# Optimization experiments

Measured on AMD Instinct MI355X. Metric: run time of the kernel, lower is better.

The kernel has to match this reference:

```python
import jax, jax.numpy as jnp
import numpy as np

B, T, C = 4, 4096, 512
H = 64           # head_size
GRAN = 128       # staircase granularity


def staircase_mask(t, g):
    # tril OR block-diagonal blocks of size g (the staircase fills the upper
    # triangle inside each gxg diagonal block)
    i = jnp.arange(t)
    return (i[:, None] >= i[None, :]) | ((i[:, None] // g) == (i[None, :] // g))


def setup_inputs() -> dict:
    key = jax.random.key(0)
    kx, kk, kq, kv = jax.random.split(key, 4)
    scale = 0.02
    return {
        "x": jax.random.normal(kx, (B, T, C), dtype=jnp.float32),
        "Wk": jax.random.normal(kk, (C, H), dtype=jnp.float32) * scale,
        "Wq": jax.random.normal(kq, (C, H), dtype=jnp.float32) * scale,
        "Wv": jax.random.normal(kv, (C, H), dtype=jnp.float32) * scale,
    }


def reference(x, Wk, Wq, Wv):
    # single head of self-attention with staircase mask (dropout off / eval mode)
    k = x @ Wk          # [B,T,H]
    q = x @ Wq          # [B,T,H]
    v = x @ Wv          # [B,T,H]
    wei = jnp.einsum("bth,bsh->bts", q, k) * (H ** -0.5)   # [B,T,T]
    mask = staircase_mask(T, GRAN)                           # [T,T] bool
    wei = jnp.where(mask, wei, -jnp.inf)
    wei = jax.nn.softmax(wei, axis=-1)
    out = jnp.einsum("bts,bsh->bth", wei, v)                 # [B,T,H]
    return out
```

## Files before the change

kernel.cpp:

```cpp
#include <hip/hip_runtime.h>

typedef unsigned short u16;
typedef unsigned int u32;
typedef unsigned long long u64;
typedef __attribute__((ext_vector_type(8))) short short8;
typedef __attribute__((ext_vector_type(4))) float f32x4;

#define T_ 4096

#if __has_builtin(__builtin_amdgcn_exp2f)
#define EXP2F(x) __builtin_amdgcn_exp2f(x)
#else
#define EXP2F(x) exp2f(x)
#endif

__device__ __forceinline__ u16 f2bf(float f) {
    unsigned u = __float_as_uint(f);
    u += 0x7FFFu + ((u >> 16) & 1u);
    return (u16)(u >> 16);
}

__global__ __launch_bounds__(256) void wtrans_kernel(
    const float* __restrict__ Wq, const float* __restrict__ Wk,
    const float* __restrict__ Wv, u16* __restrict__ WTf)
{
    const int tid  = blockIdx.x * 256 + threadIdx.x;
    const int frag = tid >> 6;
    const int lane = tid & 63;
    const int ng   = frag >> 4;
    const int kc   = frag & 15;
    const int m    = ng >> 2;
    const float* W = (m == 0) ? Wq : (m == 1) ? Wk : Wv;
    const int h  = (ng & 3) * 16 + (lane & 15);
    const int c0 = kc * 32 + (lane >> 4) * 8;
    short8 v;
    #pragma unroll
    for (int j = 0; j < 8; ++j)
        v[j] = (short)f2bf(W[(c0 + j) * 64 + h]);
    *(short8*)(WTf + (size_t)frag * 512 + lane * 8) = v;
}

__global__ __launch_bounds__(256) void proj_kernel(
    const float* __restrict__ x, const u16* __restrict__ WTf,
    u16* __restrict__ Qf, u16* __restrict__ Kf, u16* __restrict__ Vf)
{
    __shared__ u16 xs[32 * 520];
    const int lane = threadIdx.x & 63;
    const int w    = threadIdx.x >> 6;
    const int l16  = lane & 15;
    const int quad = lane >> 4;
    const int rowbase = blockIdx.x * 32;

    #pragma unroll
    for (int it = 0; it < 16; ++it) {
        int f   = threadIdx.x + it * 256;
        int row = f >> 7;
        int c4  = (f & 127) * 4;
        f32x4 a = *(const f32x4*)(x + (size_t)(rowbase + row) * 512 + c4);
        unsigned lo = (unsigned)f2bf(a[0]) | ((unsigned)f2bf(a[1]) << 16);
        unsigned hi = (unsigned)f2bf(a[2]) | ((unsigned)f2bf(a[3]) << 16);
        *(uint2*)(xs + row * 520 + c4) = make_uint2(lo, hi);
    }
    __syncthreads();

    f32x4 acc[2][3];
    #pragma unroll
    for (int g = 0; g < 2; ++g)
        for (int nt = 0; nt < 3; ++nt) acc[g][nt] = (f32x4){0.f, 0.f, 0.f, 0.f};

    const int ng0 = w * 3;
    const u16* a0 = xs + l16 * 520 + quad * 8;
    const u16* a1 = xs + (16 + l16) * 520 + quad * 8;
    const u16* wb = WTf + (size_t)(ng0 * 16) * 512 + lane * 8;

    #pragma unroll 4
    for (int kc = 0; kc < 16; ++kc) {
        short8 af0 = *(const short8*)(a0 + kc * 32);
        short8 af1 = *(const short8*)(a1 + kc * 32);
        #pragma unroll
        for (int nt = 0; nt < 3; ++nt) {
            short8 bf = *(const short8*)(wb + (size_t)(nt * 16 + kc) * 512);
            acc[0][nt] = __builtin_amdgcn_mfma_f32_16x16x32_bf16(af0, bf, acc[0][nt], 0, 0, 0);
            acc[1][nt] = __builtin_amdgcn_mfma_f32_16x16x32_bf16(af1, bf, acc[1][nt], 0, 0, 0);
        }
    }

    __syncthreads();
    #pragma unroll
    for (int g = 0; g < 2; ++g) {
        #pragma unroll
        for (int nt = 0; nt < 3; ++nt) {
            int ng = ng0 + nt;
            if (ng < 8) {
                int ng4 = ng & 3;
                u16* ib = xs + ((ng < 4) ? 0 : 2048) + g * 1024 + (ng4 >> 1) * 512
                             + ((ng4 & 1) * 2 + (l16 >> 3)) * 128 + (l16 & 7);
                #pragma unroll
                for (int i = 0; i < 4; ++i)
                    ib[(quad * 4 + i) * 8] = f2bf(acc[g][nt][i]);
            } else {
                int nt2   = ng - 8;
                int quadV = 2 * g + (quad >> 1);
                int jv4   = (quad & 1) * 4;
                unsigned lo = (unsigned)f2bf(acc[g][nt][0]) | ((unsigned)f2bf(acc[g][nt][1]) << 16);
                unsigned hi = (unsigned)f2bf(acc[g][nt][2]) | ((unsigned)f2bf(acc[g][nt][3]) << 16);
                *(uint2*)(xs + 4096 + nt2 * 512 + quadV * 128 + l16 * 8 + jv4) = make_uint2(lo, hi);
            }
        }
    }
    __syncthreads();
    const int t   = threadIdx.x;
    const int bat = rowbase >> 12;
    const int tloc = rowbase & 4095;
    const int tb0 = tloc >> 4;
    const int kt  = tloc >> 7;
    const int ks  = (tloc >> 5) & 3;
    short8 vq = *(short8*)(xs + t * 8);
    short8 vk = *(short8*)(xs + 2048 + t * 8);
    short8 vv = *(short8*)(xs + 4096 + t * 8);
    *(short8*)(Qf + (size_t)(bat * 256 + tb0) * 1024 + t * 8) = vq;
    *(short8*)(Kf + (size_t)(bat * 256 + tb0) * 1024 + t * 8) = vk;
    *(short8*)(Vf + (size_t)((bat * 32 + kt) * 4 + ks) * 2048 + t * 8) = vv;
}

__global__ __launch_bounds__(256, 4) void attn_kernel(
    const u16* __restrict__ Qf, const u16* __restrict__ Kf,
    const u16* __restrict__ Vf, u32* __restrict__ pnum,
    float* __restrict__ pden, int CH, int S_bat)
{
    const int w    = threadIdx.x >> 6;
    const int lane = threadIdx.x & 63;
    const int l16  = lane & 15;
    const int qd   = lane >> 4;
    const int xcd  = blockIdx.x & 7;
    const int bat  = xcd >> 1;
    const int tw   = ((blockIdx.x >> 3) * 2 + (xcd & 1)) * 4 + w;

    int A = 31, pre = 0, cc = 1;
    for (;;) {
        cc = (A + CH) / CH;
        int cnt = 4 * cc;
        if (tw < pre + cnt) break;
        pre += cnt; --A;
    }
    const int r    = tw - pre;
    const int c    = r >> 2;
    const int b_   = r & 3;
    const int nkt  = A + 1;
    const int q32  = 4 * A + b_;
    const int kt0  = c * CH;
    const int kt1  = min(kt0 + CH, nkt);
    const int slot = bat * S_bat + tw;

    short8 aq[2][2];
    #pragma unroll
    for (int g = 0; g < 2; ++g)
        #pragma unroll
        for (int f = 0; f < 2; ++f)
            aq[g][f] = *(const short8*)(Qf
                + ((size_t)((bat * 256 + q32 * 2 + g) * 2 + f)) * 512 + lane * 8);

    f32x4 acc[2][4];
    float den[2] = {0.f, 0.f};
    #pragma unroll
    for (int g = 0; g < 2; ++g)
        for (int n = 0; n < 4; ++n) acc[g][n] = (f32x4){0.f, 0.f, 0.f, 0.f};

    for (int kt = kt0; kt < kt1; ++kt) {
        const u16* kfb = Kf + ((size_t)(bat * 256 + kt * 8) * 2) * 512 + lane * 8;
        const u16* vfb = Vf + ((size_t)((bat * 32 + kt) * 16)) * 512 + lane * 8;
        #pragma unroll
        for (int ks = 0; ks < 4; ++ks) {
            u32 pk[2][2][2];
            #pragma unroll
            for (int b = 0; b < 2; ++b) {
                int nt = 2 * ks + b;
                short8 k0 = *(const short8*)(kfb + (size_t)nt * 1024);
                short8 k1 = *(const short8*)(kfb + (size_t)nt * 1024 + 512);
                #pragma unroll
                for (int g = 0; g < 2; ++g) {
                    f32x4 st = (f32x4){0.f, 0.f, 0.f, 0.f};
                    st = __builtin_amdgcn_mfma_f32_16x16x32_bf16(k0, aq[g][0], st, 0, 0, 0);
                    st = __builtin_amdgcn_mfma_f32_16x16x32_bf16(k1, aq[g][1], st, 0, 0, 0);
                    float p0 = EXP2F(st[0] * 0.18033688f);
                    float p1 = EXP2F(st[1] * 0.18033688f);
                    float p2 = EXP2F(st[2] * 0.18033688f);
                    float p3 = EXP2F(st[3] * 0.18033688f);
                    u32 q01 = __builtin_amdgcn_perm(__float_as_uint(p1), __float_as_uint(p0), 0x07060302u);
                    u32 q23 = __builtin_amdgcn_perm(__float_as_uint(p3), __float_as_uint(p2), 0x07060302u);
                    den[g] += __uint_as_float(q01 << 16) + __uint_as_float(q01 & 0xffff0000u)
                            + __uint_as_float(q23 << 16) + __uint_as_float(q23 & 0xffff0000u);
                    pk[b][g][0] = q01;
                    pk[b][g][1] = q23;
                }
            }
            short8 ap[2];
            #pragma unroll
            for (int g = 0; g < 2; ++g) {
                u32 av[4];
                #pragma unroll
                for (int d = 0; d < 4; ++d) {
                    int h  = d & 1;
                    int qs = (qd & 1) * 2 + (d >> 1);
                    int sl = qs * 16 + l16;
                    int t0 = __shfl((int)pk[0][g][h], sl);
                    int t1 = __shfl((int)pk[1][g][h], sl);
                    av[d] = (qd < 2) ? (u32)t0 : (u32)t1;
                }
                union { u32 u[4]; short8 s8; } cv;
                cv.u[0] = av[0]; cv.u[1] = av[1]; cv.u[2] = av[2]; cv.u[3] = av[3];
                ap[g] = cv.s8;
            }
            #pragma unroll
            for (int nt2 = 0; nt2 < 4; ++nt2) {
                short8 av = *(const short8*)(vfb + (size_t)(ks * 4 + nt2) * 512);
                acc[0][nt2] = __builtin_amdgcn_mfma_f32_16x16x32_bf16(av, ap[0], acc[0][nt2], 0, 0, 0);
                acc[1][nt2] = __builtin_amdgcn_mfma_f32_16x16x32_bf16(av, ap[1], acc[1][nt2], 0, 0, 0);
            }
        }
    }

    u32* np = pnum + (size_t)slot * 1024;
    #pragma unroll
    for (int g = 0; g < 2; ++g)
        #pragma unroll
        for (int nt2 = 0; nt2 < 4; ++nt2) {
            u32 lo = (u32)f2bf(acc[g][nt2][0]) | ((u32)f2bf(acc[g][nt2][1]) << 16);
            u32 hi = (u32)f2bf(acc[g][nt2][2]) | ((u32)f2bf(acc[g][nt2][3]) << 16);
            u64 val = (u64)lo | ((u64)hi << 32);
            __builtin_nontemporal_store(val, (u64*)(np + (g * 4 + nt2) * 128 + lane * 2));
        }
    #pragma unroll
    for (int g = 0; g < 2; ++g) {
        float d = den[g];
        d += __shfl_xor(d, 16);
        d += __shfl_xor(d, 32);
        if (lane < 16)
            __builtin_nontemporal_store(d, &pden[(size_t)slot * 32 + g * 16 + l16]);
    }
}

__global__ __launch_bounds__(256) void fin_kernel(
    const u32* __restrict__ pnum, const float* __restrict__ pden,
    float* __restrict__ out, int CH, int S_bat)
{
    __shared__ float rden[32];
    const int bq  = blockIdx.x;
    const int bat = bq >> 7;
    const int q32 = bq & 127;
    const int A = q32 >> 2, b = q32 & 3;
    int pre = 0;
    for (int j = 31; j > A; --j) pre += 4 * ((j + CH) / CH);
    const int cc   = (A + CH) / CH;
    const int base = bat * S_bat + pre + b;

    if (threadIdx.x < 32) {
        float d = 0.f;
        for (int ci = 0; ci < cc; ++ci)
            d += pden[(size_t)(base + 4 * ci) * 32 + threadIdx.x];
        rden[threadIdx.x] = 1.0f / d;
    }
    __syncthreads();

    const int m   = threadIdx.x >> 3;
    const int g   = m >> 4;
    const int l16 = m & 15;
    const int h0  = (threadIdx.x & 7) * 8;
    const int nt2 = h0 >> 4;
    const int q0  = (h0 >> 2) & 3;
    const int off = (g * 4 + nt2) * 128 + q0 * 32 + l16 * 2;

    float sv[8];
    #pragma unroll
    for (int e = 0; e < 8; ++e) sv[e] = 0.f;
    for (int ci = 0; ci < cc; ++ci) {
        const u32* sp = pnum + (size_t)(base + 4 * ci) * 1024 + off;
        uint2 a  = *(const uint2*)(sp);
        uint2 bb = *(const uint2*)(sp + 32);
        u32 vals[4] = {a.x, a.y, bb.x, bb.y};
        #pragma unroll
        for (int e = 0; e < 4; ++e) {
            sv[2 * e]     += __uint_as_float(vals[e] << 16);
            sv[2 * e + 1] += __uint_as_float(vals[e] & 0xFFFF0000u);
        }
    }
    const float rd = rden[m];
    float* op = out + (size_t)(bat * T_ + q32 * 32 + m) * 64 + h0;
    f32x4 r0, r1;
    #pragma unroll
    for (int i = 0; i < 4; ++i) { r0[i] = sv[i] * rd; r1[i] = sv[4 + i] * rd; }
    *(f32x4*)(op)     = r0;
    *(f32x4*)(op + 4) = r1;
}

extern "C" void kernel_launch(void* const* d_in, const int* in_sizes, int n_in,
                              void* d_out, int out_size, void* d_ws, size_t ws_size,
                              hipStream_t stream)
{
    const float* x  = (const float*)d_in[0];
    const float* Wk = (const float*)d_in[1];
    const float* Wq = (const float*)d_in[2];
    const float* Wv = (const float*)d_in[3];
    float* out = (float*)d_out;

    u16* ws  = (u16*)d_ws;
    u16* WTf = ws;
    u16* Qf  = ws + 131072;
    u16* Kf  = Qf + 1048576;
    u16* Vf  = Kf + 1048576;
    const size_t core_elems = 131072 + 3 * 1048576;

    auto Sof = [](int CH) { int S = 0; for (int A = 0; A < 32; ++A) S += 4 * ((A + CH) / CH); return S; };
    int CH = 2, S = Sof(2);
    size_t need = core_elems * 2 + (size_t)4 * S * (1024 * 4 + 32 * 4);
    if (ws_size < need) { CH = 4; S = Sof(4); need = core_elems * 2 + (size_t)4 * S * (1024 * 4 + 32 * 4); }
    if (ws_size < need) { CH = 8; S = Sof(8); }
    u32*   pnum = (u32*)(ws + core_elems);
    float* pden = (float*)(pnum + (size_t)4 * S * 1024);

    wtrans_kernel<<<48, 256, 0, stream>>>(Wq, Wk, Wv, WTf);
    proj_kernel<<<512, 256, 0, stream>>>(x, WTf, Qf, Kf, Vf);
    attn_kernel<<<S, 256, 0, stream>>>(Qf, Kf, Vf, pnum, pden, CH, S);
    fin_kernel<<<512, 256, 0, stream>>>(pnum, pden, out, CH, S);
}
```

Baseline: 130.9 us.

## Fold softmax scale into Q projection, shrink proj tiles, use finer attention split

The projection kernel now handles 16 rows per block instead of 32, reading x straight from global memory into MFMA fragments and skipping the LDS staging copy. It launches twice as many blocks and uses a smaller shared image. The softmax scale (log2e/sqrt(H)) is now applied to Q when it is written, which removes a multiply per score from the attention inner loop. The attention split chunk drops from 2 to 1 key tile, giving more blocks and more partial results for fin_kernel to combine. This needs more workspace and costs extra reduction work. Rounding scaled Q to bf16 slightly changes numerics.

```diff
diff --git a/kernel.cpp b/kernel.cpp
--- a/kernel.cpp
+++ b/kernel.cpp
@@ -7,6 +7,7 @@
 typedef __attribute__((ext_vector_type(4))) float f32x4;
 
 #define T_ 4096
+#define QSCALE 0.18033688f
 
 #if __has_builtin(__builtin_amdgcn_exp2f)
 #define EXP2F(x) __builtin_amdgcn_exp2f(x)
@@ -44,83 +45,72 @@
     const float* __restrict__ x, const u16* __restrict__ WTf,
     u16* __restrict__ Qf, u16* __restrict__ Kf, u16* __restrict__ Vf)
 {
-    __shared__ u16 xs[32 * 520];
-    const int lane = threadIdx.x & 63;
-    const int w    = threadIdx.x >> 6;
+    __shared__ u16 img[3072];
+    const int t    = threadIdx.x;
+    const int lane = t & 63;
+    const int w    = t >> 6;
     const int l16  = lane & 15;
     const int quad = lane >> 4;
-    const int rowbase = blockIdx.x * 32;
-
-    #pragma unroll
-    for (int it = 0; it < 16; ++it) {
-        int f   = threadIdx.x + it * 256;
-        int row = f >> 7;
-        int c4  = (f & 127) * 4;
-        f32x4 a = *(const f32x4*)(x + (size_t)(rowbase + row) * 512 + c4);
-        unsigned lo = (unsigned)f2bf(a[0]) | ((unsigned)f2bf(a[1]) << 16);
-        unsigned hi = (unsigned)f2bf(a[2]) | ((unsigned)f2bf(a[3]) << 16);
-        *(uint2*)(xs + row * 520 + c4) = make_uint2(lo, hi);
-    }
-    __syncthreads();
-
-    f32x4 acc[2][3];
-    #pragma unroll
-    for (int g = 0; g < 2; ++g)
-        for (int nt = 0; nt < 3; ++nt) acc[g][nt] = (f32x4){0.f, 0.f, 0.f, 0.f};
-
-    const int ng0 = w * 3;
-    const u16* a0 = xs + l16 * 520 + quad * 8;
-    const u16* a1 = xs + (16 + l16) * 520 + quad * 8;
-    const u16* wb = WTf + (size_t)(ng0 * 16) * 512 + lane * 8;
+    const int rowbase = blockIdx.x * 16;
+    const int bat  = rowbase >> 12;
+    const int tloc = rowbase & 4095;
+
+    f32x4 acc[3];
+    #pragma unroll
+    for (int nt = 0; nt < 3; ++nt) acc[nt] = (f32x4){0.f, 0.f, 0.f, 0.f};
+
+    const float* xp = x + (size_t)(rowbase + l16) * 512 + quad * 8;
+    const u16*   wb = WTf + (size_t)(w * 3 * 16) * 512 + lane * 8;
 
     #pragma unroll 4
     for (int kc = 0; kc < 16; ++kc) {
-        short8 af0 = *(const short8*)(a0 + kc * 32);
-        short8 af1 = *(const short8*)(a1 + kc * 32);
+        f32x4 a0 = *(const f32x4*)(xp + kc * 32);
+        f32x4 a1 = *(const f32x4*)(xp + kc * 32 + 4);
+        short8 af;
+        af[0] = (short)f2bf(a0[0]); af[1] = (short)f2bf(a0[1]);
+        af[2] = (short)f2bf(a0[2]); af[3] = (short)f2bf(a0[3]);
+        af[4] = (short)f2bf(a1[0]); af[5] = (short)f2bf(a1[1]);
+        af[6] = (short)f2bf(a1[2]); af[7] = (short)f2bf(a1[3]);
         #pragma unroll
         for (int nt = 0; nt < 3; ++nt) {
             short8 bf = *(const short8*)(wb + (size_t)(nt * 16 + kc) * 512);
-            acc[0][nt] = __builtin_amdgcn_mfma_f32_16x16x32_bf16(af0, bf, acc[0][nt], 0, 0, 0);
-            acc[1][nt] = __builtin_amdgcn_mfma_f32_16x16x32_bf16(af1, bf, acc[1][nt], 0, 0, 0);
-        }
-    }
-
+            acc[nt] = __builtin_amdgcn_mfma_f32_16x16x32_bf16(af, bf, acc[nt], 0, 0, 0);
+        }
+    }
+
+    #pragma unroll
+    for (int nt = 0; nt < 3; ++nt) {
+        int ng = w * 3 + nt;
+        if (ng < 8) {
+            int ng4  = ng & 3;
+            float sc = (ng < 4) ? QSCALE : 1.0f;
+            u16* ib  = img + ((ng < 4) ? 0 : 1024) + (ng4 >> 1) * 512
+                          + ((ng4 & 1) * 2 + (l16 >> 3)) * 128 + (l16 & 7);
+            #pragma unroll
+            for (int i = 0; i < 4; ++i)
+                ib[(quad * 4 + i) * 8] = f2bf(acc[nt][i] * sc);
+        } else {
+            int nt2  = ng - 8;
+            unsigned lo = (unsigned)f2bf(acc[nt][0]) | ((unsigned)f2bf(acc[nt][1]) << 16);
+            unsigned hi = (unsigned)f2bf(acc[nt][2]) | ((unsigned)f2bf(acc[nt][3]) << 16);
+            *(uint2*)(img + 2048 + nt2 * 256 + (quad >> 1) * 128 + l16 * 8
+                          + (quad & 1) * 4) = make_uint2(lo, hi);
+        }
+    }
     __syncthreads();
-    #pragma unroll
-    for (int g = 0; g < 2; ++g) {
-        #pragma unroll
-        for (int nt = 0; nt < 3; ++nt) {
-            int ng = ng0 + nt;
-            if (ng < 8) {
-                int ng4 = ng & 3;
-                u16* ib = xs + ((ng < 4) ? 0 : 2048) + g * 1024 + (ng4 >> 1) * 512
-                             + ((ng4 & 1) * 2 + (l16 >> 3)) * 128 + (l16 & 7);
-                #pragma unroll
-                for (int i = 0; i < 4; ++i)
-                    ib[(quad * 4 + i) * 8] = f2bf(acc[g][nt][i]);
-            } else {
-                int nt2   = ng - 8;
-                int quadV = 2 * g + (quad >> 1);
-                int jv4   = (quad & 1) * 4;
-                unsigned lo = (unsigned)f2bf(acc[g][nt][0]) | ((unsigned)f2bf(acc[g][nt][1]) << 16);
-                unsigned hi = (unsigned)f2bf(acc[g][nt][2]) | ((unsigned)f2bf(acc[g][nt][3]) << 16);
-                *(uint2*)(xs + 4096 + nt2 * 512 + quadV * 128 + l16 * 8 + jv4) = make_uint2(lo, hi);
-            }
-        }
-    }
-    __syncthreads();
-    const int t   = threadIdx.x;
-    const int bat = rowbase >> 12;
-    const int tloc = rowbase & 4095;
-    const int tb0 = tloc >> 4;
-    const int kt  = tloc >> 7;
-    const int ks  = (tloc >> 5) & 3;
-    short8 vq = *(short8*)(xs + t * 8);
-    short8 vk = *(short8*)(xs + 2048 + t * 8);
-    short8 vv = *(short8*)(xs + 4096 + t * 8);
-    *(short8*)(Qf + (size_t)(bat * 256 + tb0) * 1024 + t * 8) = vq;
-    *(short8*)(Kf + (size_t)(bat * 256 + tb0) * 1024 + t * 8) = vk;
-    *(short8*)(Vf + (size_t)((bat * 32 + kt) * 4 + ks) * 2048 + t * 8) = vv;
+
+    const int tb   = tloc >> 4;
+    const int kt   = tloc >> 7;
+    const int ks   = (tloc >> 5) & 3;
+    const int half = (tloc >> 4) & 1;
+    uint2 vq = *(uint2*)(img + t * 4);
+    uint2 vk = *(uint2*)(img + 1024 + t * 4);
+    uint2 vv = *(uint2*)(img + 2048 + t * 4);
+    *(uint2*)(Qf + (size_t)(bat * 256 + tb) * 1024 + t * 4) = vq;
+    *(uint2*)(Kf + (size_t)(bat * 256 + tb) * 1024 + t * 4) = vk;
+    const int nt2c = t >> 6;
+    *(uint2*)(Vf + (size_t)((bat * 32 + kt) * 4 + ks) * 2048
+                 + nt2c * 512 + half * 256 + (t & 63) * 4) = vv;
 }
 
 __global__ __launch_bounds__(256, 4) void attn_kernel(
@@ -182,10 +172,10 @@
                     f32x4 st = (f32x4){0.f, 0.f, 0.f, 0.f};
                     st = __builtin_amdgcn_mfma_f32_16x16x32_bf16(k0, aq[g][0], st, 0, 0, 0);
                     st = __builtin_amdgcn_mfma_f32_16x16x32_bf16(k1, aq[g][1], st, 0, 0, 0);
-                    float p0 = EXP2F(st[0] * 0.18033688f);
-                    float p1 = EXP2F(st[1] * 0.18033688f);
-                    float p2 = EXP2F(st[2] * 0.18033688f);
-                    float p3 = EXP2F(st[3] * 0.18033688f);
+                    float p0 = EXP2F(st[0]);
+                    float p1 = EXP2F(st[1]);
+                    float p2 = EXP2F(st[2]);
+                    float p3 = EXP2F(st[3]);
                     u32 q01 = __builtin_amdgcn_perm(__float_as_uint(p1), __float_as_uint(p0), 0x07060302u);
                     u32 q23 = __builtin_amdgcn_perm(__float_as_uint(p3), __float_as_uint(p2), 0x07060302u);
                     den[g] += __uint_as_float(q01 << 16) + __uint_as_float(q01 & 0xffff0000u)
@@ -311,15 +301,15 @@
     const size_t core_elems = 131072 + 3 * 1048576;
 
     auto Sof = [](int CH) { int S = 0; for (int A = 0; A < 32; ++A) S += 4 * ((A + CH) / CH); return S; };
-    int CH = 2, S = Sof(2);
+    int CH = 1, S = Sof(1);
     size_t need = core_elems * 2 + (size_t)4 * S * (1024 * 4 + 32 * 4);
-    if (ws_size < need) { CH = 4; S = Sof(4); need = core_elems * 2 + (size_t)4 * S * (1024 * 4 + 32 * 4); }
-    if (ws_size < need) { CH = 8; S = Sof(8); }
+    if (ws_size < need) { CH = 2; S = Sof(2); need = core_elems * 2 + (size_t)4 * S * (1024 * 4 + 32 * 4); }
+    if (ws_size < need) { CH = 4; S = Sof(4); }
     u32*   pnum = (u32*)(ws + core_elems);
     float* pden = (float*)(pnum + (size_t)4 * S * 1024);
 
     wtrans_kernel<<<48, 256, 0, stream>>>(Wq, Wk, Wv, WTf);
-    proj_kernel<<<512, 256, 0, stream>>>(x, WTf, Qf, Kf, Vf);
+    proj_kernel<<<1024, 256, 0, stream>>>(x, WTf, Qf, Kf, Vf);
     attn_kernel<<<S, 256, 0, stream>>>(Qf, Kf, Vf, pnum, pden, CH, S);
     fin_kernel<<<512, 256, 0, stream>>>(pnum, pden, out, CH, S);
 }
```

New measurement: 154.2 us. 1.18x slower.
